# Kernel optimization log

Hardware: AMD Instinct MI355X
Metric: run time of the kernel (lower is better)

Reference implementation:

```python
import jax, jax.numpy as jnp
import numpy as np

B, LQ, LKV, LT, C, H = 4, 1024, 1344, 320, 768, 12
DH = C // H
SCALE = DH ** -0.5
HID = 4 * C
EPS = 1e-5


def _ln(x, g, b):
    m = jnp.mean(x, axis=-1, keepdims=True)
    v = jnp.mean((x - m) ** 2, axis=-1, keepdims=True)
    return (x - m) * jax.lax.rsqrt(v + EPS) * g + b


def setup_inputs() -> dict:
    key = jax.random.key(0)
    ks = jax.random.split(key, 16)
    s = lambda k, shape, sc=0.02: jax.random.normal(k, shape, dtype=jnp.float32) * sc
    return {
        "tem_mask": s(ks[0], (B, LT, C), 1.0),
        "q": s(ks[1], (B, LQ, C), 1.0),
        "kv": s(ks[2], (B, LKV, C), 1.0),
        "attn_pos": s(ks[3], (1, H, LQ, LKV), 1.0),
        "ln1q_g": jnp.ones((C,)), "ln1q_b": jnp.zeros((C,)),
        "ln1kv_g": jnp.ones((C,)), "ln1kv_b": jnp.zeros((C,)),
        "Wq": s(ks[4], (C, C)), "bq": jnp.zeros((C,)),
        "Wkv": s(ks[5], (C, 2 * C)), "bkv": jnp.zeros((2 * C,)),
        "Wp": s(ks[6], (C, C)), "bp": jnp.zeros((C,)),
        "ln2_g": jnp.ones((C,)), "ln2_b": jnp.zeros((C,)),
        "W1": s(ks[7], (C, HID)), "b1": jnp.zeros((HID,)),
        "W2": s(ks[8], (HID, C)), "b2": jnp.zeros((C,)),
    }


def reference(tem_mask, q, kv, attn_pos, ln1q_g, ln1q_b, ln1kv_g, ln1kv_b,
              Wq, bq, Wkv, bkv, Wp, bp, ln2_g, ln2_b, W1, b1, W2, b2):
    qn = _ln(q, ln1q_g, ln1q_b)
    kvn = _ln(kv, ln1kv_g, ln1kv_b)
    # projections (attn_pos_encoding_only branch)
    qh = (qn @ Wq + bq).reshape(B, LQ, H, DH).transpose(0, 2, 1, 3)  # (B,H,Lq,Dh)
    kvp = kvn @ Wkv + bkv
    k, v = kvp[:, :, :C], kvp[:, :, C:]
    v = v.at[:, :LT, :].add(tem_mask)  # add template mask to template tokens
    kh = k.reshape(B, LKV, H, DH).transpose(0, 2, 1, 3)
    vh = v.reshape(B, LKV, H, DH).transpose(0, 2, 1, 3)
    attn = jnp.einsum('bhqd,bhkd->bhqk', qh, kh) * SCALE + attn_pos
    attn = jax.nn.softmax(attn, axis=-1)
    x = jnp.einsum('bhqk,bhkd->bhqd', attn, vh)
    x = x.transpose(0, 2, 1, 3).reshape(B, LQ, C)
    x = x @ Wp + bp
    q = q + x  # residual 1 (drop_path = Identity, dropout eval)
    h = _ln(q, ln2_g, ln2_b)
    h = jax.nn.gelu(h @ W1 + b1, approximate=False)
    h = h @ W2 + b2
    return q + h
```

## Files before the change

### kernel.cpp

```cpp
#include <hip/hip_runtime.h>
#include <hip/hip_bf16.h>
#include <math.h>

typedef __bf16 bf16x8 __attribute__((ext_vector_type(8)));
typedef float f32x4 __attribute__((ext_vector_type(4)));

__device__ __forceinline__ __hip_bfloat16 f2bf(float v){ return __float2bfloat16(v); }

__device__ __forceinline__ void gload16(const void* g, void* l){
  __builtin_amdgcn_global_load_lds(
      (const __attribute__((address_space(1))) void*)g,
      (__attribute__((address_space(3))) void*)l, 16, 0, 0);
}

__global__ void transpose_all(const float* __restrict__ Wq, const float* __restrict__ Wkv,
                              const float* __restrict__ Wp, const float* __restrict__ W1,
                              const float* __restrict__ W2,
                              __hip_bfloat16* __restrict__ oq, __hip_bfloat16* __restrict__ okv,
                              __hip_bfloat16* __restrict__ op_, __hip_bfloat16* __restrict__ o1,
                              __hip_bfloat16* __restrict__ o2){
  __shared__ float tile[32][33];
  const int bid = blockIdx.x;
  const float* in; __hip_bfloat16* out; int K, N, local;
  if(bid < 576)        { in=Wq;  out=oq;  K=768;  N=768;  local=bid; }
  else if(bid < 1728)  { in=Wkv; out=okv; K=768;  N=1536; local=bid-576; }
  else if(bid < 2304)  { in=Wp;  out=op_; K=768;  N=768;  local=bid-1728; }
  else if(bid < 4608)  { in=W1;  out=o1;  K=768;  N=3072; local=bid-2304; }
  else                 { in=W2;  out=o2;  K=3072; N=768;  local=bid-4608; }
  const int nbx = N/32;
  const int n0 = (local % nbx)*32, k0 = (local / nbx)*32;
  int tx = threadIdx.x, ty = threadIdx.y;
#pragma unroll
  for(int i=0;i<4;i++) tile[ty+i*8][tx] = in[(size_t)(k0+ty+i*8)*N + n0+tx];
  __syncthreads();
#pragma unroll
  for(int i=0;i<4;i++) out[(size_t)(n0+ty+i*8)*K + k0+tx] = f2bf(tile[tx][ty+i*8]);
}

__device__ __forceinline__ void ln_body(const float* rp, const float* g, const float* b,
                                        __hip_bfloat16* op, int t){
  float x0 = rp[t], x1 = rp[t+256], x2 = rp[t+512];
  float s = x0+x1+x2, ss = x0*x0+x1*x1+x2*x2;
#pragma unroll
  for(int o=32;o>0;o>>=1){ s += __shfl_down(s,o); ss += __shfl_down(ss,o); }
  __shared__ float red[10];
  if((t&63)==0){ red[t>>6]=s; red[4+(t>>6)]=ss; }
  __syncthreads();
  if(t==0){
    float S=red[0]+red[1]+red[2]+red[3], SS=red[4]+red[5]+red[6]+red[7];
    float m=S*(1.f/768.f);
    red[8]=m; red[9]=SS*(1.f/768.f)-m*m;
  }
  __syncthreads();
  float m=red[8], r=rsqrtf(red[9]+1e-5f);
  op[t]     = f2bf((x0-m)*r*g[t]     + b[t]);
  op[t+256] = f2bf((x1-m)*r*g[t+256] + b[t+256]);
  op[t+512] = f2bf((x2-m)*r*g[t+512] + b[t+512]);
}

__global__ __launch_bounds__(256) void ln_qkv(const float* __restrict__ q, const float* __restrict__ kv,
    const float* __restrict__ qg, const float* __restrict__ qb,
    const float* __restrict__ kg, const float* __restrict__ kb2,
    __hip_bfloat16* __restrict__ qn, __hip_bfloat16* __restrict__ kvn){
  int row = blockIdx.x, t = threadIdx.x;
  if(row < 4096) ln_body(q + (size_t)row*768, qg, qb, qn + (size_t)row*768, t);
  else { row -= 4096; ln_body(kv + (size_t)row*768, kg, kb2, kvn + (size_t)row*768, t); }
}

__global__ __launch_bounds__(256) void ln_kernel(const float* __restrict__ in,
    const float* __restrict__ g, const float* __restrict__ b,
    __hip_bfloat16* __restrict__ out){
  int row = blockIdx.x, t = threadIdx.x;
  ln_body(in + (size_t)row*768, g, b, out + (size_t)row*768, t);
}

template<int BM, int BN, int EPI>
__global__ __launch_bounds__(256) void gemm_gl(
    const __hip_bfloat16* __restrict__ A, const __hip_bfloat16* __restrict__ BT,
    const float* __restrict__ bias, int M, int N, int K,
    void* __restrict__ out, const void* __restrict__ aux0, void* __restrict__ out2){
  constexpr int WR = (BM==128 || BN==64) ? 2 : 1;
  constexpr int WC = 4/WR;
  constexpr int MF = BM/(WR*16);
  constexpr int NF = BN/(WC*16);
  constexpr int NBUF = (BM==64 && BN==64) ? 3 : 2;
  constexpr int LPS = BM/32 + BN/32;
  __shared__ char sA[NBUF][BM*128];
  __shared__ char sB[NBUF][BN*128];
  const int tid = threadIdx.x;
  const int l = tid & 63, w = tid >> 6;
  const int lg = l >> 4, li = l & 15;
  const int wrow = (WR==2) ? (w>>1)*(BM/2) : 0;
  const int wcol = (WC==2) ? (w&1)*(BN/2) : w*(BN/4);
  const int bm = blockIdx.x * BM;
  const int bn = blockIdx.y * BN;
  const int arow = w*(BM/4) + (l>>3);
  const int brow = w*(BN/4) + (l>>3);
  const int scol = ((((l&7)*16) ^ ((l>>3)<<4)) >> 1);

  auto stage = [&](int buf, int kt){
    const int k0 = kt*64;
#pragma unroll
    for(int i=0;i<BM/32;i++)
      gload16(A  + (size_t)(bm+arow+i*8)*K + k0 + scol, sA[buf] + (w*(BM/4))*128 + i*1024);
#pragma unroll
    for(int i=0;i<BN/32;i++)
      gload16(BT + (size_t)(bn+brow+i*8)*K + k0 + scol, sB[buf] + (w*(BN/4))*128 + i*1024);
  };

  f32x4 acc[MF][NF] = {};
  const int nk = K >> 6;

  if constexpr(NBUF==3){
    stage(0, 0);
    stage(1, 1);
  } else {
    stage(0, 0);
    __syncthreads();
  }

  for(int kt=0; kt<nk; ++kt){
    const char *cA, *cB;
    if constexpr(NBUF==3){
      if(kt+1 < nk) asm volatile("s_waitcnt vmcnt(%0)" :: "i"(LPS) : "memory");
      else          asm volatile("s_waitcnt vmcnt(0)" ::: "memory");
      __builtin_amdgcn_s_barrier();
      if(kt+2 < nk) stage((kt+2)%3, kt+2);
      cA = sA[kt%3]; cB = sB[kt%3];
    } else {
      const int cur = kt & 1;
      if(kt+1 < nk) stage(cur^1, kt+1);
      cA = sA[cur]; cB = sB[cur];
    }
#pragma unroll
    for(int kk=0;kk<2;kk++){
      const int kb = kk*64 + lg*16;
      bf16x8 af[MF], bfr[NF];
#pragma unroll
      for(int m=0;m<MF;m++){
        int row = wrow+m*16+li;
        af[m] = *(const bf16x8*)(cA + row*128 + (kb ^ ((row&7)<<4)));
      }
#pragma unroll
      for(int n=0;n<NF;n++){
        int row = wcol+n*16+li;
        bfr[n] = *(const bf16x8*)(cB + row*128 + (kb ^ ((row&7)<<4)));
      }
#pragma unroll
      for(int m=0;m<MF;m++)
#pragma unroll
        for(int n=0;n<NF;n++)
          acc[m][n] = __builtin_amdgcn_mfma_f32_16x16x32_bf16(af[m], bfr[n], acc[m][n],0,0,0);
    }
    if constexpr(NBUF==2) __syncthreads();
  }
#pragma unroll
  for(int m=0;m<MF;m++){
#pragma unroll
    for(int n=0;n<NF;n++){
      if constexpr(EPI==1){
        const int col = bn + wcol + n*16 + li;
        const int row0 = bm + wrow + m*16 + lg*4;
        const int bb = row0 / 1344, ii = row0 % 1344;
        if(col < 768){
#pragma unroll
          for(int r=0;r<4;r++)
            ((__hip_bfloat16*)out)[(size_t)(row0+r)*768 + col] = f2bf(acc[m][n][r] + bias[col]);
        } else {
          const int c = col - 768, hh = c >> 6, d = c & 63;
          __hip_bfloat16 tmp[4];
#pragma unroll
          for(int r=0;r<4;r++){
            float v = acc[m][n][r] + bias[col];
            if(ii < 320) v += ((const float*)aux0)[((size_t)bb*320 + ii + r)*768 + c];
            tmp[r] = f2bf(v);
          }
          *(uint2*)((__hip_bfloat16*)out2 + ((size_t)(bb*12+hh)*64 + d)*1344 + ii) = *(const uint2*)tmp;
        }
      } else {
#pragma unroll
        for(int r=0;r<4;r++){
          int row = bm + wrow + m*16 + lg*4 + r;
          int col = bn + wcol + n*16 + li;
          float v = acc[m][n][r] + bias[col];
          if constexpr(EPI==0){
            ((__hip_bfloat16*)out)[(size_t)row*N + col] = f2bf(v * 0.125f);
          } else if constexpr(EPI==2){
            v += ((const float*)aux0)[(size_t)row*N + col];
            ((float*)out)[(size_t)row*N + col] = v;
          } else if constexpr(EPI==3){
            float u = v*(0.7978845608f + 0.0356774081f*v*v);
            float e = __expf(-2.f*fabsf(u));
            float th = (1.f - e)/(1.f + e);
            th = (u < 0.f) ? -th : th;
            ((__hip_bfloat16*)out)[(size_t)row*N + col] = f2bf(0.5f*v*(1.f+th));
          } else {
            v += ((const float*)aux0)[(size_t)row*N + col];
            ((float*)out)[(size_t)row*N + col] = v;
          }
        }
      }
    }
  }
}

__global__ __launch_bounds__(256) void attn_kernel(
    const __hip_bfloat16* __restrict__ qh,
    const __hip_bfloat16* __restrict__ kb,
    const __hip_bfloat16* __restrict__ vt,
    const float* __restrict__ pos,
    __hip_bfloat16* __restrict__ xo){
  __shared__ char sK[2][8192];
  __shared__ char sV[2][8192];
  __shared__ char sP[4][2048];
  const int bid = blockIdx.x;
  const int qt = bid & 15, h = (bid >> 4) % 12, b = bid / 192;
  const int q0 = qt * 64;
  const int tid = threadIdx.x;
  const int l = tid & 63, w = tid >> 6;
  const int lg = l >> 4, li = l & 15;

  const int srow = w*16 + (l>>3);
  const int soff = (((l&7)*16) ^ ((l>>3)<<4)) >> 1;
  const __hip_bfloat16* ksrc = kb + ((size_t)b*1344 + srow)*768 + h*64 + soff;
  const __hip_bfloat16* vsrc = vt + ((size_t)(b*12+h)*64 + srow)*1344 + soff;

  bf16x8 aq[2];
  {
    const char* qp = (const char*)(qh + ((size_t)(b*1024 + q0 + w*16 + li))*768 + h*64);
    aq[0] = *(const bf16x8*)(qp + lg*16);
    aq[1] = *(const bf16x8*)(qp + 64 + lg*16);
  }
  bf16x8 ones;
#pragma unroll
  for(int i=0;i<8;i++) ones[i] = (__bf16)1.0f;
  const size_t posbase = ((size_t)h*1024 + q0 + w*16 + lg*4)*1344 + li;

  f32x4 accO[4] = {};
  f32x4 accL = {};
  float mrun[4];
#pragma unroll
  for(int r=0;r<4;r++) mrun[r] = -1e30f;

  auto stage = [&](int buf, int t){
    const size_t ko = (size_t)t*64*768;
    const size_t vo = (size_t)t*64;
    gload16(ksrc + ko,          sK[buf] + w*2048);
    gload16(ksrc + ko + 8*768,  sK[buf] + w*2048 + 1024);
    gload16(vsrc + vo,          sV[buf] + w*2048);
    gload16(vsrc + vo + 8*1344, sV[buf] + w*2048 + 1024);
  };
  auto ldpos = [&](int t, float (&pr)[4][4]){
    const float* pp = pos + posbase + (size_t)t*64;
#pragma unroll
    for(int n=0;n<4;n++)
#pragma unroll
      for(int r=0;r<4;r++)
        pr[n][r] = __builtin_nontemporal_load(pp + (size_t)r*1344 + n*16);
  };

  float pA[4][4], pB[4][4];
  ldpos(0, pA);
  stage(0, 0);
  __syncthreads();

  char* sPw = sP[w];

  auto body = [&](int t, float (&posr)[4][4], float (&npos)[4][4]){
    const int cur = t & 1;
    const bool more = (t < 20);
    f32x4 accS[4] = {};
    __builtin_amdgcn_s_setprio(1);
#pragma unroll
    for(int kk=0; kk<2; ++kk){
      const int kbyte = kk*64 + lg*16;
#pragma unroll
      for(int n=0;n<4;n++){
        int row = n*16 + li;
        bf16x8 bkf = *(const bf16x8*)(sK[cur] + row*128 + (kbyte ^ ((row&7)<<4)));
        accS[n] = __builtin_amdgcn_mfma_f32_16x16x32_bf16(aq[kk], bkf, accS[n], 0,0,0);
      }
    }
    __builtin_amdgcn_s_setprio(0);
    if(more) stage(cur^1, t+1);
    asm volatile("" ::: "memory");
    if(more) ldpos(t+1, npos);

    float p[4][4], mt[4];
#pragma unroll
    for(int r=0;r<4;r++) mt[r] = -1e30f;
#pragma unroll
    for(int n=0;n<4;n++)
#pragma unroll
      for(int r=0;r<4;r++){
        float s = accS[n][r] + posr[n][r];
        p[n][r] = s;
        mt[r] = fmaxf(mt[r], s);
      }
    bool need = false;
#pragma unroll
    for(int r=0;r<4;r++) need |= (mt[r] > mrun[r] + 8.f);
    if(__any(need)){
#pragma unroll
      for(int r=0;r<4;r++){
#pragma unroll
        for(int o=1;o<16;o<<=1) mt[r] = fmaxf(mt[r], __shfl_xor(mt[r], o));
        float mnew = fmaxf(mrun[r], mt[r]);
        float sf = __expf(mrun[r]-mnew);
        mrun[r] = mnew;
        accL[r] *= sf;
#pragma unroll
        for(int n=0;n<4;n++) accO[n][r] *= sf;
      }
    }
#pragma unroll
    for(int n=0;n<4;n++)
#pragma unroll
      for(int r=0;r<4;r++) p[n][r] = __expf(p[n][r]-mrun[r]);
#pragma unroll
    for(int n=0;n<4;n++)
#pragma unroll
      for(int r=0;r<4;r++){
        int qi = lg*4 + r, kj = n*16 + li;
        *(__hip_bfloat16*)(sPw + qi*128 + ((kj*2) ^ ((qi&7)<<4))) = f2bf(p[n][r]);
      }
    __builtin_amdgcn_s_setprio(1);
#pragma unroll
    for(int kk=0; kk<2; ++kk){
      const int kbyte = kk*64 + lg*16;
      bf16x8 pa = *(const bf16x8*)(sPw + li*128 + (kbyte ^ ((li&7)<<4)));
      accL = __builtin_amdgcn_mfma_f32_16x16x32_bf16(pa, ones, accL, 0,0,0);
#pragma unroll
      for(int n=0;n<4;n++){
        int d = n*16 + li;
        bf16x8 bvf = *(const bf16x8*)(sV[cur] + d*128 + (kbyte ^ ((d&7)<<4)));
        accO[n] = __builtin_amdgcn_mfma_f32_16x16x32_bf16(pa, bvf, accO[n], 0,0,0);
      }
    }
    __builtin_amdgcn_s_setprio(0);
    if(more){
      asm volatile("s_waitcnt vmcnt(16)" ::: "memory");
      __builtin_amdgcn_s_barrier();
    }
  };

  for(int tt=0; tt<10; ++tt){
    body(2*tt,   pA, pB);
    body(2*tt+1, pB, pA);
  }
  body(20, pA, pB);

#pragma unroll
  for(int n=0;n<4;n++)
#pragma unroll
    for(int r=0;r<4;r++){
      int row = b*1024 + q0 + w*16 + lg*4 + r;
      int col = h*64 + n*16 + li;
      xo[(size_t)row*768 + col] = f2bf(accO[n][r] / accL[r]);
    }
}

extern "C" void kernel_launch(void* const* d_in, const int* in_sizes, int n_in,
                              void* d_out, int out_size, void* d_ws, size_t ws_size,
                              hipStream_t stream){
  const float* tem   = (const float*)d_in[0];
  const float* qin   = (const float*)d_in[1];
  const float* kvin  = (const float*)d_in[2];
  const float* pos   = (const float*)d_in[3];
  const float* ln1qg = (const float*)d_in[4];
  const float* ln1qb = (const float*)d_in[5];
  const float* ln1kg = (const float*)d_in[6];
  const float* ln1kb = (const float*)d_in[7];
  const float* Wq    = (const float*)d_in[8];
  const float* bq    = (const float*)d_in[9];
  const float* Wkv   = (const float*)d_in[10];
  const float* bkv   = (const float*)d_in[11];
  const float* Wp    = (const float*)d_in[12];
  const float* bp    = (const float*)d_in[13];
  const float* ln2g  = (const float*)d_in[14];
  const float* ln2b  = (const float*)d_in[15];
  const float* W1    = (const float*)d_in[16];
  const float* b1    = (const float*)d_in[17];
  const float* W2    = (const float*)d_in[18];
  const float* b2    = (const float*)d_in[19];

  char* ws = (char*)d_ws; size_t off = 0;
  auto alloc = [&](size_t n){ char* p = ws + off; off = (off + n + 255) & ~(size_t)255; return p; };
  __hip_bfloat16* WqT  = (__hip_bfloat16*)alloc((size_t)768*768*2);
  __hip_bfloat16* WkvT = (__hip_bfloat16*)alloc((size_t)1536*768*2);
  __hip_bfloat16* WpT  = (__hip_bfloat16*)alloc((size_t)768*768*2);
  __hip_bfloat16* W1T  = (__hip_bfloat16*)alloc((size_t)3072*768*2);
  __hip_bfloat16* W2T  = (__hip_bfloat16*)alloc((size_t)768*3072*2);
  __hip_bfloat16* qn   = (__hip_bfloat16*)alloc((size_t)4096*768*2);
  char* poolBase = alloc((size_t)5376*768*2*3 + (size_t)4096*768*2);
  __hip_bfloat16* kvn  = (__hip_bfloat16*)poolBase;
  __hip_bfloat16* kbuf = kvn  + (size_t)5376*768;
  __hip_bfloat16* vt   = kbuf + (size_t)5376*768;
  __hip_bfloat16* qhb  = vt   + (size_t)5376*768;
  __hip_bfloat16* xat  = (__hip_bfloat16*)alloc((size_t)4096*768*2);
  float*          x1f  = (float*)alloc((size_t)4096*768*4);
  __hip_bfloat16* hln  = qn;
  __hip_bfloat16* h1   = kvn;

  transpose_all<<<6912, dim3(32,8), 0, stream>>>(Wq, Wkv, Wp, W1, W2, WqT, WkvT, WpT, W1T, W2T);
  ln_qkv<<<4096+5376, 256, 0, stream>>>(qin, kvin, ln1qg, ln1qb, ln1kg, ln1kb, qn, kvn);

  gemm_gl<64,64,0>  <<<dim3(64, 12), 256, 0, stream>>>(qn,  WqT,  bq,  4096, 768,  768,  qhb, nullptr, nullptr);
  gemm_gl<128,128,1><<<dim3(42, 12), 256, 0, stream>>>(kvn, WkvT, bkv, 5376, 1536, 768,  kbuf, tem, vt);

  attn_kernel<<<768, 256, 0, stream>>>(qhb, kbuf, vt, pos, xat);

  gemm_gl<64,64,2>  <<<dim3(64, 12), 256, 0, stream>>>(xat, WpT,  bp,  4096, 768,  768,  x1f, qin, nullptr);
  ln_kernel<<<4096, 256, 0, stream>>>(x1f, ln2g, ln2b, hln);
  gemm_gl<128,128,3><<<dim3(32, 24), 256, 0, stream>>>(hln, W1T,  b1,  4096, 3072, 768,  h1, nullptr, nullptr);
  gemm_gl<64,64,4>  <<<dim3(64, 12), 256, 0, stream>>>(h1,  W2T,  b2,  4096, 768,  3072, (float*)d_out, x1f, nullptr);
}
```

Baseline: 222.9 us.

## Split attention over KV into two partitions with reduce kernel; merge prep kernels

Attention now splits the 21 KV tiles into two halves handled by separate blocks, doubling the grid from 768 to 1536 workgroups. Each block writes unnormalized bf16 partial outputs plus row sums and maxima, and a new reduce kernel combines them with log-sum-exp rescaling. The weight transpose and the first layernorm are also merged into one launch. This targets low occupancy on a large-CU GPU and one launch gap, at the cost of an extra kernel, extra memory traffic and bf16 rounding of the partial outputs.

```diff
diff --git a/kernel.cpp b/kernel.cpp
--- a/kernel.cpp
+++ b/kernel.cpp
@@ -11,30 +11,6 @@
   __builtin_amdgcn_global_load_lds(
       (const __attribute__((address_space(1))) void*)g,
       (__attribute__((address_space(3))) void*)l, 16, 0, 0);
-}
-
-__global__ void transpose_all(const float* __restrict__ Wq, const float* __restrict__ Wkv,
-                              const float* __restrict__ Wp, const float* __restrict__ W1,
-                              const float* __restrict__ W2,
-                              __hip_bfloat16* __restrict__ oq, __hip_bfloat16* __restrict__ okv,
-                              __hip_bfloat16* __restrict__ op_, __hip_bfloat16* __restrict__ o1,
-                              __hip_bfloat16* __restrict__ o2){
-  __shared__ float tile[32][33];
-  const int bid = blockIdx.x;
-  const float* in; __hip_bfloat16* out; int K, N, local;
-  if(bid < 576)        { in=Wq;  out=oq;  K=768;  N=768;  local=bid; }
-  else if(bid < 1728)  { in=Wkv; out=okv; K=768;  N=1536; local=bid-576; }
-  else if(bid < 2304)  { in=Wp;  out=op_; K=768;  N=768;  local=bid-1728; }
-  else if(bid < 4608)  { in=W1;  out=o1;  K=768;  N=3072; local=bid-2304; }
-  else                 { in=W2;  out=o2;  K=3072; N=768;  local=bid-4608; }
-  const int nbx = N/32;
-  const int n0 = (local % nbx)*32, k0 = (local / nbx)*32;
-  int tx = threadIdx.x, ty = threadIdx.y;
-#pragma unroll
-  for(int i=0;i<4;i++) tile[ty+i*8][tx] = in[(size_t)(k0+ty+i*8)*N + n0+tx];
-  __syncthreads();
-#pragma unroll
-  for(int i=0;i<4;i++) out[(size_t)(n0+ty+i*8)*K + k0+tx] = f2bf(tile[tx][ty+i*8]);
 }
 
 __device__ __forceinline__ void ln_body(const float* rp, const float* g, const float* b,
@@ -58,13 +34,40 @@
   op[t+512] = f2bf((x2-m)*r*g[t+512] + b[t+512]);
 }
 
-__global__ __launch_bounds__(256) void ln_qkv(const float* __restrict__ q, const float* __restrict__ kv,
+__global__ __launch_bounds__(256) void prep_kernel(
+    const float* __restrict__ Wq, const float* __restrict__ Wkv,
+    const float* __restrict__ Wp, const float* __restrict__ W1,
+    const float* __restrict__ W2,
+    __hip_bfloat16* __restrict__ oq, __hip_bfloat16* __restrict__ okv,
+    __hip_bfloat16* __restrict__ op_, __hip_bfloat16* __restrict__ o1,
+    __hip_bfloat16* __restrict__ o2,
+    const float* __restrict__ q, const float* __restrict__ kv,
     const float* __restrict__ qg, const float* __restrict__ qb,
     const float* __restrict__ kg, const float* __restrict__ kb2,
     __hip_bfloat16* __restrict__ qn, __hip_bfloat16* __restrict__ kvn){
-  int row = blockIdx.x, t = threadIdx.x;
-  if(row < 4096) ln_body(q + (size_t)row*768, qg, qb, qn + (size_t)row*768, t);
-  else { row -= 4096; ln_body(kv + (size_t)row*768, kg, kb2, kvn + (size_t)row*768, t); }
+  const int bid = blockIdx.x;
+  const int tid = threadIdx.x;
+  if(bid < 6912){
+    __shared__ float tile[32][33];
+    const float* in; __hip_bfloat16* out; int K, N, local;
+    if(bid < 576)        { in=Wq;  out=oq;  K=768;  N=768;  local=bid; }
+    else if(bid < 1728)  { in=Wkv; out=okv; K=768;  N=1536; local=bid-576; }
+    else if(bid < 2304)  { in=Wp;  out=op_; K=768;  N=768;  local=bid-1728; }
+    else if(bid < 4608)  { in=W1;  out=o1;  K=768;  N=3072; local=bid-2304; }
+    else                 { in=W2;  out=o2;  K=3072; N=768;  local=bid-4608; }
+    const int nbx = N/32;
+    const int n0 = (local % nbx)*32, k0 = (local / nbx)*32;
+    const int tx = tid & 31, ty = tid >> 5;
+#pragma unroll
+    for(int i=0;i<4;i++) tile[ty+i*8][tx] = in[(size_t)(k0+ty+i*8)*N + n0+tx];
+    __syncthreads();
+#pragma unroll
+    for(int i=0;i<4;i++) out[(size_t)(n0+ty+i*8)*K + k0+tx] = f2bf(tile[tx][ty+i*8]);
+  } else {
+    int row = bid - 6912;
+    if(row < 4096) ln_body(q + (size_t)row*768, qg, qb, qn + (size_t)row*768, tid);
+    else { row -= 4096; ln_body(kv + (size_t)row*768, kg, kb2, kvn + (size_t)row*768, tid); }
+  }
 }
 
 __global__ __launch_bounds__(256) void ln_kernel(const float* __restrict__ in,
@@ -209,13 +212,19 @@
     const __hip_bfloat16* __restrict__ kb,
     const __hip_bfloat16* __restrict__ vt,
     const float* __restrict__ pos,
-    __hip_bfloat16* __restrict__ xo){
+    __hip_bfloat16* __restrict__ po,
+    float* __restrict__ pl,
+    float* __restrict__ pm){
   __shared__ char sK[2][8192];
   __shared__ char sV[2][8192];
   __shared__ char sP[4][2048];
   const int bid = blockIdx.x;
-  const int qt = bid & 15, h = (bid >> 4) % 12, b = bid / 192;
+  const int s = bid & 1;
+  const int part = bid >> 1;
+  const int qt = part & 15, h = (part >> 4) % 12, b = part / 192;
   const int q0 = qt * 64;
+  const int tstart = s ? 11 : 0;
+  const int tcnt   = s ? 10 : 11;
   const int tid = threadIdx.x;
   const int l = tid & 63, w = tid >> 6;
   const int lg = l >> 4, li = l & 15;
@@ -260,15 +269,15 @@
   };
 
   float pA[4][4], pB[4][4];
-  ldpos(0, pA);
-  stage(0, 0);
+  ldpos(tstart, pA);
+  stage(0, tstart);
   __syncthreads();
 
   char* sPw = sP[w];
 
   auto body = [&](int t, float (&posr)[4][4], float (&npos)[4][4]){
     const int cur = t & 1;
-    const bool more = (t < 20);
+    const bool more = (t+1 < tcnt);
     f32x4 accS[4] = {};
     __builtin_amdgcn_s_setprio(1);
 #pragma unroll
@@ -282,9 +291,9 @@
       }
     }
     __builtin_amdgcn_s_setprio(0);
-    if(more) stage(cur^1, t+1);
+    if(more) stage(cur^1, tstart + t + 1);
     asm volatile("" ::: "memory");
-    if(more) ldpos(t+1, npos);
+    if(more) ldpos(tstart + t + 1, npos);
 
     float p[4][4], mt[4];
 #pragma unroll
@@ -293,9 +302,9 @@
     for(int n=0;n<4;n++)
 #pragma unroll
       for(int r=0;r<4;r++){
-        float s = accS[n][r] + posr[n][r];
-        p[n][r] = s;
-        mt[r] = fmaxf(mt[r], s);
+        float s2 = accS[n][r] + posr[n][r];
+        p[n][r] = s2;
+        mt[r] = fmaxf(mt[r], s2);
       }
     bool need = false;
 #pragma unroll
@@ -344,20 +353,47 @@
     }
   };
 
-  for(int tt=0; tt<10; ++tt){
-    body(2*tt,   pA, pB);
-    body(2*tt+1, pB, pA);
-  }
-  body(20, pA, pB);
-
+  for(int t=0; t<tcnt; ++t){
+    if(t & 1) body(t, pB, pA);
+    else      body(t, pA, pB);
+  }
+
+  __hip_bfloat16* Ob = po + (size_t)bid*4096;
 #pragma unroll
   for(int n=0;n<4;n++)
 #pragma unroll
+    for(int r=0;r<4;r++)
+      Ob[(w*16 + lg*4 + r)*64 + n*16 + li] = f2bf(accO[n][r]);
+  if(li == 0){
+#pragma unroll
     for(int r=0;r<4;r++){
-      int row = b*1024 + q0 + w*16 + lg*4 + r;
-      int col = h*64 + n*16 + li;
-      xo[(size_t)row*768 + col] = f2bf(accO[n][r] / accL[r]);
-    }
+      pl[bid*64 + w*16 + lg*4 + r] = accL[r];
+      pm[bid*64 + w*16 + lg*4 + r] = mrun[r];
+    }
+  }
+}
+
+__global__ __launch_bounds__(256) void attn_reduce(
+    const __hip_bfloat16* __restrict__ po, const float* __restrict__ pl,
+    const float* __restrict__ pm, __hip_bfloat16* __restrict__ xo){
+  const int part = blockIdx.x;
+  const int qt = part & 15, h = (part >> 4) % 12, b = part / 192;
+  const int tid = threadIdx.x;
+  const int q = tid >> 2, dd = (tid & 3) * 16;
+  const float m0 = pm[(part*2+0)*64 + q], m1 = pm[(part*2+1)*64 + q];
+  const float L0 = pl[(part*2+0)*64 + q], L1 = pl[(part*2+1)*64 + q];
+  const float mx = fmaxf(m0, m1);
+  const float a0 = __expf(m0 - mx), a1 = __expf(m1 - mx);
+  const float inv = 1.f / (L0*a0 + L1*a1);
+  const __hip_bfloat16* O0 = po + ((size_t)(part*2+0))*4096 + q*64 + dd;
+  const __hip_bfloat16* O1 = po + ((size_t)(part*2+1))*4096 + q*64 + dd;
+  __hip_bfloat16 tmp[16];
+#pragma unroll
+  for(int i=0;i<16;i++)
+    tmp[i] = f2bf((__bfloat162float(O0[i])*a0 + __bfloat162float(O1[i])*a1) * inv);
+  __hip_bfloat16* op = xo + ((size_t)(b*1024 + qt*64 + q))*768 + h*64 + dd;
+  *(uint4*)op       = *(const uint4*)tmp;
+  *(uint4*)(op + 8) = *(const uint4*)(tmp + 8);
 }
 
 extern "C" void kernel_launch(void* const* d_in, const int* in_sizes, int n_in,
@@ -401,14 +437,18 @@
   float*          x1f  = (float*)alloc((size_t)4096*768*4);
   __hip_bfloat16* hln  = qn;
   __hip_bfloat16* h1   = kvn;
-
-  transpose_all<<<6912, dim3(32,8), 0, stream>>>(Wq, Wkv, Wp, W1, W2, WqT, WkvT, WpT, W1T, W2T);
-  ln_qkv<<<4096+5376, 256, 0, stream>>>(qin, kvin, ln1qg, ln1qb, ln1kg, ln1kb, qn, kvn);
+  __hip_bfloat16* po   = (__hip_bfloat16*)x1f;
+  float*          pl   = (float*)qn;
+  float*          pm   = pl + 1536*64;
+
+  prep_kernel<<<16384, 256, 0, stream>>>(Wq, Wkv, Wp, W1, W2, WqT, WkvT, WpT, W1T, W2T,
+                                         qin, kvin, ln1qg, ln1qb, ln1kg, ln1kb, qn, kvn);
 
   gemm_gl<64,64,0>  <<<dim3(64, 12), 256, 0, stream>>>(qn,  WqT,  bq,  4096, 768,  768,  qhb, nullptr, nullptr);
   gemm_gl<128,128,1><<<dim3(42, 12), 256, 0, stream>>>(kvn, WkvT, bkv, 5376, 1536, 768,  kbuf, tem, vt);
 
-  attn_kernel<<<768, 256, 0, stream>>>(qhb, kbuf, vt, pos, xat);
+  attn_kernel<<<1536, 256, 0, stream>>>(qhb, kbuf, vt, pos, po, pl, pm);
+  attn_reduce<<<768, 256, 0, stream>>>(po, pl, pm, xat);
 
   gemm_gl<64,64,2>  <<<dim3(64, 12), 256, 0, stream>>>(xat, WpT,  bp,  4096, 768,  768,  x1f, qin, nullptr);
   ln_kernel<<<4096, 256, 0, stream>>>(x1f, ln2g, ln2b, hln);
```

Measured after the change: 231.9 us. +4.0%, slower.
